# Performance work log

Measured on AMD Instinct MI355X. Metric: run time of the kernel, lower is better.

## Reference

```python
import jax, jax.numpy as jnp
import numpy as np

EMB, HEADS = 1024, 16
HEAD_DIM = EMB // HEADS


def _linear(x, W, b):
    # torch nn.Linear convention: x @ W.T + b, W: [out, in]
    return jnp.einsum('bse,oe->bso', x, W) + b


def setup_inputs() -> dict:
    key = jax.random.key(0)
    ks = jax.random.split(key, 11)
    B, S = 2, 2048
    sc = 1.0 / np.sqrt(EMB)
    inp = {
        'x': jax.random.normal(ks[0], (B, S, EMB), dtype=jnp.float32),
        'y': jax.random.normal(ks[1], (B, S, EMB), dtype=jnp.float32),
        'mask': jnp.ones((B, S, S), dtype=jnp.int32),
        'Wq': jax.random.normal(ks[2], (EMB, EMB), dtype=jnp.float32) * sc,
        'bq': jax.random.normal(ks[3], (EMB,), dtype=jnp.float32) * sc,
        'Wk': jax.random.normal(ks[4], (EMB, EMB), dtype=jnp.float32) * sc,
        'bk': jax.random.normal(ks[5], (EMB,), dtype=jnp.float32) * sc,
        'Wv': jax.random.normal(ks[6], (EMB, EMB), dtype=jnp.float32) * sc,
        'bv': jax.random.normal(ks[7], (EMB,), dtype=jnp.float32) * sc,
        'Wo': jax.random.normal(ks[8], (EMB, EMB), dtype=jnp.float32) * sc,
        'bo': jax.random.normal(ks[9], (EMB,), dtype=jnp.float32) * sc,
    }
    return inp


def reference(x, y, mask, Wq, bq, Wk, bk, Wv, bv, Wo, bo):
    B, S, _ = x.shape
    q = _linear(x, Wq, bq).reshape(B, S, HEADS, HEAD_DIM).transpose(0, 2, 1, 3)
    k = _linear(y, Wk, bk).reshape(B, -1, HEADS, HEAD_DIM).transpose(0, 2, 1, 3)
    v = _linear(y, Wv, bv).reshape(B, -1, HEADS, HEAD_DIM).transpose(0, 2, 1, 3)
    # scores: [B, H, Sq, Sk]
    score = jnp.einsum('bhqd,bhkd->bhqk', q, k) / jnp.sqrt(jnp.float32(HEAD_DIM))
    # NOTE: original torch code calls score.masked_fill(...) without assignment,
    # so the mask has no effect on the computation (faithfully ignored here).
    weights = jax.nn.softmax(score, axis=-1)
    attn = jnp.einsum('bhqk,bhkd->bhqd', weights, v)
    attn = attn.transpose(0, 2, 1, 3).reshape(B, S, EMB)
    # dropout is identity in eval mode
    return _linear(attn, Wo, bo)
```

## Files before the change

### kernel.cpp

```cpp
#include <hip/hip_runtime.h>
#include <cstdint>
#include <cstddef>

#define BB 2
#define SS 2048
#define EE 1024
#define HH 16
#define DD 64

typedef __attribute__((ext_vector_type(8))) short short8;
typedef __attribute__((ext_vector_type(4))) short shortx4;
typedef __attribute__((ext_vector_type(8))) unsigned short ushort8;
typedef __attribute__((ext_vector_type(4))) unsigned short ush4;
typedef __attribute__((ext_vector_type(4))) float floatx4;

#define MFMA32(a, b, c) __builtin_amdgcn_mfma_f32_16x16x32_bf16((a), (b), (c), 0, 0, 0)
#define MFMA16(a, b, c) __builtin_amdgcn_mfma_f32_16x16x16bf16_1k((a), (b), (c), 0, 0, 0)

#define QSCALE 0.18033688011112042f

#define G2L16(g, l)                                                        \
    __builtin_amdgcn_global_load_lds(                                      \
        (const __attribute__((address_space(1))) void*)(g),                \
        (__attribute__((address_space(3))) void*)(l), 16, 0, 0)

__device__ __forceinline__ unsigned short f2bf(float f) {
    unsigned int u = __float_as_uint(f);
    u += 0x7fffu + ((u >> 16) & 1u);
    return (unsigned short)(u >> 16);
}

__device__ __forceinline__ unsigned int pkbf(float a, float b) {
    return __builtin_amdgcn_perm(__float_as_uint(b) + 0x8000u,
                                 __float_as_uint(a) + 0x8000u, 0x07060302u);
}

__global__ __launch_bounds__(256) void k_cvt(
    const float* __restrict__ x, unsigned short* __restrict__ xb,
    const float* __restrict__ y, unsigned short* __restrict__ yb,
    const float* __restrict__ w0, unsigned short* __restrict__ d0,
    const float* __restrict__ w1, unsigned short* __restrict__ d1,
    const float* __restrict__ w2, unsigned short* __restrict__ d2,
    const float* __restrict__ w3, unsigned short* __restrict__ d3)
{
    const int g = blockIdx.y;
    if (g >= 2 && blockIdx.x >= 256) return;
    const float* s = (g == 0) ? x : (g == 1) ? y : (g == 2) ? w0
                   : (g == 3) ? w1 : (g == 4) ? w2 : w3;
    unsigned short* d = (g == 0) ? xb : (g == 1) ? yb : (g == 2) ? d0
                      : (g == 3) ? d1 : (g == 4) ? d2 : d3;
    const size_t i = ((size_t)blockIdx.x * 256 + threadIdx.x) * 16;
    floatx4 f0 = *(const floatx4*)(s + i);
    floatx4 f1 = *(const floatx4*)(s + i + 4);
    floatx4 f2 = *(const floatx4*)(s + i + 8);
    floatx4 f3 = *(const floatx4*)(s + i + 12);
    ushort8 o0, o1;
#pragma unroll
    for (int j = 0; j < 4; ++j) { o0[j] = f2bf(f0[j]); o0[j + 4] = f2bf(f1[j]); }
#pragma unroll
    for (int j = 0; j < 4; ++j) { o1[j] = f2bf(f2[j]); o1[j + 4] = f2bf(f3[j]); }
    *(ushort8*)(d + i) = o0;
    *(ushort8*)(d + i + 8) = o1;
}

template <int MT, int OMODE>
__device__ __forceinline__ void gemm_body(
    const unsigned short* __restrict__ A, const unsigned short* __restrict__ W,
    const float* __restrict__ bias, void* __restrict__ Cv, float oscale,
    int m0, int n0,
    unsigned short* As0, unsigned short* As1, unsigned short* As2,
    unsigned short* Bs0, unsigned short* Bs1, unsigned short* Bs2)
{
    constexpr int K = 1024, N = 1024, LDT = 32;
    constexpr int MFR = MT / 32;
    constexpr int KEEP = (MT == 128) ? 8 : 6;
    const int t = threadIdx.x;
    const int lane = t & 63, w = t >> 6;
    const int q = lane >> 4, c = lane & 15;
    const int wm = w & 1, wn = w >> 1;
    const int lr = lane >> 2, lc = (lane & 3) * 8;

    const unsigned short* gA0 = A + (size_t)(m0 + w * (MT / 4) + lr) * K + lc;
    const unsigned short* gA1 = gA0 + 16 * K;
    const unsigned short* gB0 = W + (size_t)(n0 + w * 32 + lr) * K + lc;
    const unsigned short* gB1 = gB0 + 16 * K;
    unsigned short* lA0 = As0 + (w * (MT / 4)) * LDT;
    unsigned short* lA1 = As1 + (w * (MT / 4)) * LDT;
    unsigned short* lA2 = As2 + (w * (MT / 4)) * LDT;
    unsigned short* lB0 = Bs0 + (w * 32) * LDT;
    unsigned short* lB1 = Bs1 + (w * 32) * LDT;
    unsigned short* lB2 = Bs2 + (w * 32) * LDT;

    floatx4 acc[MFR][4] = {};

    auto compute = [&](const unsigned short* Ah, const unsigned short* Bh) {
        short8 af[MFR], bfr[4];
#pragma unroll
        for (int mi = 0; mi < MFR; ++mi)
            af[mi] = *(const short8*)
                &Ah[(wm * (MFR * 16) + mi * 16 + c) * LDT + q * 8];
#pragma unroll
        for (int ni = 0; ni < 4; ++ni)
            bfr[ni] = *(const short8*)
                &Bh[(wn * 64 + ni * 16 + c) * LDT + q * 8];
#pragma unroll
        for (int mi = 0; mi < MFR; ++mi)
#pragma unroll
            for (int ni = 0; ni < 4; ++ni)
                acc[mi][ni] = MFMA32(af[mi], bfr[ni], acc[mi][ni]);
    };

    auto stage = [&](int nk, unsigned short* lA, unsigned short* lB) {
        G2L16(gA0 + nk, lA);
        if constexpr (MT == 128) G2L16(gA1 + nk, lA + 16 * LDT);
        G2L16(gB0 + nk, lB);
        G2L16(gB1 + nk, lB + 16 * LDT);
    };

    auto phase = [&](int knext, unsigned short* lAn, unsigned short* lBn,
                     const unsigned short* Ac, const unsigned short* Bc) {
        __builtin_amdgcn_s_barrier();
        stage(knext & (K - 1), lAn, lBn);
        asm volatile("s_waitcnt vmcnt(%0)" :: "n"(KEEP) : "memory");
        __builtin_amdgcn_s_barrier();
        __builtin_amdgcn_sched_barrier(0);
        compute(Ac, Bc);
    };

    stage(0, lA0, lB0);
    stage(32, lA1, lB1);

    for (int g = 0; g < 10; ++g) {
        const int kb = g * 96;
        phase(kb +  64, lA2, lB2, As0, Bs0);
        phase(kb +  96, lA0, lB0, As1, Bs1);
        phase(kb + 128, lA1, lB1, As2, Bs2);
    }
    phase(1056, lA2, lB2, As0, Bs0);
    phase(1088, lA0, lB0, As1, Bs1);
    asm volatile("s_waitcnt vmcnt(0)" ::: "memory");

#pragma unroll
    for (int ni = 0; ni < 4; ++ni) {
        const int col = n0 + wn * 64 + ni * 16 + c;
        const float bv = bias[col];
#pragma unroll
        for (int mi = 0; mi < MFR; ++mi)
#pragma unroll
            for (int r = 0; r < 4; ++r) {
                const int row = m0 + wm * (MFR * 16) + mi * 16 + q * 4 + r;
                const float v = (acc[mi][ni][r] + bv) * oscale;
                if constexpr (OMODE == 0) {
                    ((unsigned short*)Cv)[(size_t)row * N + col] = f2bf(v);
                } else if constexpr (OMODE == 1) {
                    const int b = row >> 11, s = row & 2047;
                    ((unsigned short*)Cv)[((size_t)(b * 1024 + col)) * SS + s] = f2bf(v);
                } else {
                    ((float*)Cv)[(size_t)row * N + col] = v;
                }
            }
    }
}

__global__ __launch_bounds__(256) void k_gemm_qkv(
    const unsigned short* __restrict__ x, const unsigned short* __restrict__ y,
    const unsigned short* __restrict__ Wq, const float* __restrict__ bq,
    const unsigned short* __restrict__ Wk, const float* __restrict__ bk,
    const unsigned short* __restrict__ Wv, const float* __restrict__ bv,
    unsigned short* __restrict__ Q, unsigned short* __restrict__ Ko,
    unsigned short* __restrict__ Vt)
{
    __shared__ __align__(16) unsigned short As0[128 * 32], As1[128 * 32],
                                            As2[128 * 32];
    __shared__ __align__(16) unsigned short Bs0[128 * 32], Bs1[128 * 32],
                                            Bs2[128 * 32];
    const int m0 = blockIdx.y * 128;
    const int nt = blockIdx.x;
    const int g = nt >> 3;
    const int n0 = (nt & 7) * 128;
    if (g == 0) {
        gemm_body<128, 0>(x, Wq, bq, Q, QSCALE, m0, n0,
                          As0, As1, As2, Bs0, Bs1, Bs2);
    } else if (g == 1) {
        gemm_body<128, 0>(y, Wk, bk, Ko, 1.0f, m0, n0,
                          As0, As1, As2, Bs0, Bs1, Bs2);
    } else {
        gemm_body<128, 1>(y, Wv, bv, Vt, 1.0f, m0, n0,
                          As0, As1, As2, Bs0, Bs1, Bs2);
    }
}

__global__ __launch_bounds__(256) void k_gemm_out(
    const unsigned short* __restrict__ A, const unsigned short* __restrict__ W,
    const float* __restrict__ bias, float* __restrict__ C)
{
    __shared__ __align__(16) unsigned short As0[128 * 32], As1[128 * 32],
                                            As2[128 * 32];
    __shared__ __align__(16) unsigned short Bs0[128 * 32], Bs1[128 * 32],
                                            Bs2[128 * 32];
    gemm_body<128, 2>(A, W, bias, C, 1.0f, blockIdx.y * 128, blockIdx.x * 128,
                      As0, As1, As2, Bs0, Bs1, Bs2);
}

__global__ __launch_bounds__(512, 4) void k_attn(
    const unsigned short* __restrict__ Q, const unsigned short* __restrict__ K,
    const unsigned short* __restrict__ Vt, unsigned short* __restrict__ O)
{
    constexpr int LDK = 72;
    constexpr int TSZ = 64 * LDK + 64 * 64;
    __shared__ __align__(16) unsigned short smem[2 * 2 * TSZ];
    float* Ob = (float*)smem;

    const int bh = blockIdx.x, qt = blockIdx.y;
    const int b = bh >> 4, h = bh & 15;
    const int t = threadIdx.x, w = t >> 6;
    const int ws = w >> 2;
    const int wq = w & 3;
    const int lane = t & 63, q = lane >> 4, c = lane & 15;

    unsigned short* Sb = smem + ws * (2 * TSZ);

    short8 qb[2][2];
#pragma unroll
    for (int g = 0; g < 2; ++g) {
        const size_t qoff =
            (size_t)(b * SS + qt * 128 + wq * 32 + g * 16 + c) * EE + h * DD + q * 8;
        qb[g][0] = *(const short8*)(Q + qoff);
        qb[g][1] = *(const short8*)(Q + qoff + 32);
    }

    floatx4 o[2][4] = {};
    floatx4 lacc[2] = {};
    const shortx4 ones = {(short)0x3F80, (short)0x3F80, (short)0x3F80, (short)0x3F80};

    const int ts = t & 255;
    const int sr = ts >> 2, sp = (ts & 3) * 16;
    const int vkey = (sr & 15) << 2;
    const unsigned short* Kg =
        K + (size_t)(b * SS + ws * 1024 + sr) * EE + h * DD + sp;
    const unsigned short* Vg =
        Vt + ((size_t)bh * DD + sr) * SS + ws * 1024 + sp;

    auto put = [&](unsigned short* Ks, unsigned short* Vs,
                   ushort8 k0, ushort8 k1, ushort8 v0, ushort8 v1) {
        *(ushort8*)&Ks[sr * LDK + sp] = k0;
        *(ushort8*)&Ks[sr * LDK + sp + 8] = k1;
        *(ush4*)&Vs[sr * 64 + ((sp +  0) ^ vkey)] =
            __builtin_shufflevector(v0, v0, 0, 1, 2, 3);
        *(ush4*)&Vs[sr * 64 + ((sp +  4) ^ vkey)] =
            __builtin_shufflevector(v0, v0, 4, 5, 6, 7);
        *(ush4*)&Vs[sr * 64 + ((sp +  8) ^ vkey)] =
            __builtin_shufflevector(v1, v1, 0, 1, 2, 3);
        *(ush4*)&Vs[sr * 64 + ((sp + 12) ^ vkey)] =
            __builtin_shufflevector(v1, v1, 4, 5, 6, 7);
    };

    ushort8 rk[2][2], rv[2][2];
    {
        const ushort8* gk0 = (const ushort8*)Kg;
        rk[0][0] = gk0[0]; rk[0][1] = gk0[1];
        const ushort8* gv0 = (const ushort8*)Vg;
        rv[0][0] = gv0[0]; rv[0][1] = gv0[1];
        const ushort8* gk1 = (const ushort8*)(Kg + (size_t)64 * EE);
        rk[1][0] = gk1[0]; rk[1][1] = gk1[1];
        const ushort8* gv1 = (const ushort8*)(Vg + 64);
        rv[1][0] = gv1[0]; rv[1][1] = gv1[1];
        put(Sb, Sb + 64 * LDK, rk[0][0], rk[0][1], rv[0][0], rv[0][1]);
        asm volatile("s_waitcnt lgkmcnt(0)" ::: "memory");
    }

#pragma unroll 2
    for (int it = 0; it < 16; ++it) {
        const unsigned short* Ks = Sb + (it & 1) * TSZ;
        const unsigned short* Vs = Ks + 64 * LDK;
        __builtin_amdgcn_s_barrier();
        __builtin_amdgcn_sched_barrier(0);

        {
            const int nit = (it + 2) & 15;
            const ushort8* gk = (const ushort8*)(Kg + (size_t)nit * 64 * EE);
            rk[it & 1][0] = gk[0]; rk[it & 1][1] = gk[1];
            const ushort8* gv = (const ushort8*)(Vg + nit * 64);
            rv[it & 1][0] = gv[0]; rv[it & 1][1] = gv[1];
        }

#pragma unroll
        for (int tt = 0; tt < 4; ++tt) {
            const short8 ka0 = *(const short8*)&Ks[(tt * 16 + c) * LDK + q * 8];
            const short8 ka1 = *(const short8*)&Ks[(tt * 16 + c) * LDK + 32 + q * 8];
            shortx4 pa[2];
#pragma unroll
            for (int g = 0; g < 2; ++g) {
                floatx4 s = {0.f, 0.f, 0.f, 0.f};
                s = MFMA32(ka0, qb[g][0], s);
                s = MFMA32(ka1, qb[g][1], s);
                union { unsigned int u[2]; shortx4 v; } pk;
                pk.u[0] = pkbf(__builtin_amdgcn_exp2f(s[0]),
                               __builtin_amdgcn_exp2f(s[1]));
                pk.u[1] = pkbf(__builtin_amdgcn_exp2f(s[2]),
                               __builtin_amdgcn_exp2f(s[3]));
                pa[g] = pk.v;
            }
#pragma unroll
            for (int nd = 0; nd < 4; ++nd) {
                const shortx4 vb = *(const shortx4*)
                    &Vs[(nd * 16 + c) * 64 + (((tt * 4 + q) ^ c) << 2)];
                o[0][nd] = MFMA16(pa[0], vb, o[0][nd]);
                o[1][nd] = MFMA16(pa[1], vb, o[1][nd]);
            }
            lacc[0] = MFMA16(pa[0], ones, lacc[0]);
            lacc[1] = MFMA16(pa[1], ones, lacc[1]);
        }

        __builtin_amdgcn_sched_barrier(0);
        {
            unsigned short* Kn = Sb + ((it + 1) & 1) * TSZ;
            unsigned short* Vn = Kn + 64 * LDK;
            put(Kn, Vn, rk[(it + 1) & 1][0], rk[(it + 1) & 1][1],
                rv[(it + 1) & 1][0], rv[(it + 1) & 1][1]);
        }
        asm volatile("s_waitcnt lgkmcnt(0)" ::: "memory");
    }

    __syncthreads();
    if (ws == 1) {
#pragma unroll
        for (int g = 0; g < 2; ++g) {
#pragma unroll
            for (int nd = 0; nd < 4; ++nd)
#pragma unroll
                for (int r = 0; r < 4; ++r)
                    Ob[(wq * 32 + g * 16 + q * 4 + r) * 66 + nd * 16 + c] =
                        o[g][nd][r];
            if (c == 0) {
#pragma unroll
                for (int r = 0; r < 4; ++r)
                    Ob[(wq * 32 + g * 16 + q * 4 + r) * 66 + 64] = lacc[g][r];
            }
        }
    }
    __syncthreads();
    if (ws == 0) {
#pragma unroll
        for (int g = 0; g < 2; ++g) {
            float linv[4];
#pragma unroll
            for (int r = 0; r < 4; ++r) {
                const int rr = wq * 32 + g * 16 + q * 4 + r;
#pragma unroll
                for (int nd = 0; nd < 4; ++nd)
                    o[g][nd][r] += Ob[rr * 66 + nd * 16 + c];
                linv[r] = __builtin_amdgcn_rcpf(lacc[g][r] + Ob[rr * 66 + 64]);
            }
            const int orow = b * SS + qt * 128 + wq * 32 + g * 16;
#pragma unroll
            for (int nd = 0; nd < 4; ++nd)
#pragma unroll
                for (int r = 0; r < 4; ++r)
                    O[(size_t)(orow + q * 4 + r) * EE + h * DD + nd * 16 + c] =
                        f2bf(o[g][nd][r] * linv[r]);
        }
    }
}

extern "C" void kernel_launch(void* const* d_in, const int* in_sizes, int n_in,
                              void* d_out, int out_size, void* d_ws, size_t ws_size,
                              hipStream_t stream)
{
    const float* x  = (const float*)d_in[0];
    const float* y  = (const float*)d_in[1];
    const float* Wq = (const float*)d_in[3];
    const float* bq = (const float*)d_in[4];
    const float* Wk = (const float*)d_in[5];
    const float* bk = (const float*)d_in[6];
    const float* Wv = (const float*)d_in[7];
    const float* bv = (const float*)d_in[8];
    const float* Wo = (const float*)d_in[9];
    const float* bo = (const float*)d_in[10];
    float* out = (float*)d_out;

    char* ws = (char*)d_ws;
    const size_t SZ = (size_t)BB * SS * EE * sizeof(unsigned short);
    const size_t WZ = (size_t)EE * EE * sizeof(unsigned short);
    unsigned short* xb  = (unsigned short*)(ws);
    unsigned short* yb  = (unsigned short*)(ws + SZ);
    unsigned short* Wqb = (unsigned short*)(ws + 2 * SZ);
    unsigned short* Wkb = (unsigned short*)(ws + 2 * SZ + WZ);
    unsigned short* Wvb = (unsigned short*)(ws + 2 * SZ + 2 * WZ);
    unsigned short* Wob = (unsigned short*)(ws + 2 * SZ + 3 * WZ);
    unsigned short* Qw  = (unsigned short*)(ws + 2 * SZ + 4 * WZ);
    unsigned short* Kw  = (unsigned short*)(ws + 3 * SZ + 4 * WZ);
    unsigned short* Vtw = (unsigned short*)(ws + 4 * SZ + 4 * WZ);
    unsigned short* Aw  = (unsigned short*)(ws + 5 * SZ + 4 * WZ);
    (void)ws_size; (void)in_sizes; (void)n_in; (void)out_size;

    k_cvt<<<dim3(1024, 6), 256, 0, stream>>>(x, xb, y, yb, Wq, Wqb, Wk, Wkb,
                                             Wv, Wvb, Wo, Wob);
    k_gemm_qkv<<<dim3(24, 32), 256, 0, stream>>>(xb, yb, Wqb, bq, Wkb, bk, Wvb, bv,
                                                 Qw, Kw, Vtw);
    k_attn<<<dim3(32, 16), 512, 0, stream>>>(Qw, Kw, Vtw, Aw);
    k_gemm_out<<<dim3(8, 32), 256, 0, stream>>>(Aw, Wob, bo, out);
}
```

Measured before the change: 229.9 us.

## Fuse fp32-to-bf16 conversion into GEMM loads and drop convert kernel

Removes the standalone conversion kernel and has the projection GEMMs read fp32 activations and weights directly, converting to bf16 in registers before writing to LDS. The staging changes from async global-to-LDS triple buffering to register-staged double buffering. This eliminates a full pass over inputs and weights and the bf16 intermediate buffers, at the cost of more global read bytes per GEMM, repeated weight conversion per tile, and a less asynchronous load pipeline.

```diff
diff --git a/kernel.cpp b/kernel.cpp
--- a/kernel.cpp
+++ b/kernel.cpp
@@ -19,11 +19,6 @@
 
 #define QSCALE 0.18033688011112042f
 
-#define G2L16(g, l)                                                        \
-    __builtin_amdgcn_global_load_lds(                                      \
-        (const __attribute__((address_space(1))) void*)(g),                \
-        (__attribute__((address_space(3))) void*)(l), 16, 0, 0)
-
 __device__ __forceinline__ unsigned short f2bf(float f) {
     unsigned int u = __float_as_uint(f);
     u += 0x7fffu + ((u >> 16) & 1u);
@@ -35,120 +30,105 @@
                                  __float_as_uint(a) + 0x8000u, 0x07060302u);
 }
 
-__global__ __launch_bounds__(256) void k_cvt(
-    const float* __restrict__ x, unsigned short* __restrict__ xb,
-    const float* __restrict__ y, unsigned short* __restrict__ yb,
-    const float* __restrict__ w0, unsigned short* __restrict__ d0,
-    const float* __restrict__ w1, unsigned short* __restrict__ d1,
-    const float* __restrict__ w2, unsigned short* __restrict__ d2,
-    const float* __restrict__ w3, unsigned short* __restrict__ d3)
-{
-    const int g = blockIdx.y;
-    if (g >= 2 && blockIdx.x >= 256) return;
-    const float* s = (g == 0) ? x : (g == 1) ? y : (g == 2) ? w0
-                   : (g == 3) ? w1 : (g == 4) ? w2 : w3;
-    unsigned short* d = (g == 0) ? xb : (g == 1) ? yb : (g == 2) ? d0
-                      : (g == 3) ? d1 : (g == 4) ? d2 : d3;
-    const size_t i = ((size_t)blockIdx.x * 256 + threadIdx.x) * 16;
-    floatx4 f0 = *(const floatx4*)(s + i);
-    floatx4 f1 = *(const floatx4*)(s + i + 4);
-    floatx4 f2 = *(const floatx4*)(s + i + 8);
-    floatx4 f3 = *(const floatx4*)(s + i + 12);
-    ushort8 o0, o1;
-#pragma unroll
-    for (int j = 0; j < 4; ++j) { o0[j] = f2bf(f0[j]); o0[j + 4] = f2bf(f1[j]); }
-#pragma unroll
-    for (int j = 0; j < 4; ++j) { o1[j] = f2bf(f2[j]); o1[j + 4] = f2bf(f3[j]); }
-    *(ushort8*)(d + i) = o0;
-    *(ushort8*)(d + i + 8) = o1;
-}
-
-template <int MT, int OMODE>
-__device__ __forceinline__ void gemm_body(
-    const unsigned short* __restrict__ A, const unsigned short* __restrict__ W,
+template <int OMODE, bool AF32>
+__device__ __forceinline__ void gemm_fused(
+    const void* __restrict__ Av, const float* __restrict__ W,
     const float* __restrict__ bias, void* __restrict__ Cv, float oscale,
-    int m0, int n0,
-    unsigned short* As0, unsigned short* As1, unsigned short* As2,
-    unsigned short* Bs0, unsigned short* Bs1, unsigned short* Bs2)
+    int m0, int n0, unsigned short* As0, unsigned short* As1,
+    unsigned short* Bs0, unsigned short* Bs1)
 {
     constexpr int K = 1024, N = 1024, LDT = 32;
-    constexpr int MFR = MT / 32;
-    constexpr int KEEP = (MT == 128) ? 8 : 6;
     const int t = threadIdx.x;
     const int lane = t & 63, w = t >> 6;
     const int q = lane >> 4, c = lane & 15;
     const int wm = w & 1, wn = w >> 1;
-    const int lr = lane >> 2, lc = (lane & 3) * 8;
-
-    const unsigned short* gA0 = A + (size_t)(m0 + w * (MT / 4) + lr) * K + lc;
-    const unsigned short* gA1 = gA0 + 16 * K;
-    const unsigned short* gB0 = W + (size_t)(n0 + w * 32 + lr) * K + lc;
-    const unsigned short* gB1 = gB0 + 16 * K;
-    unsigned short* lA0 = As0 + (w * (MT / 4)) * LDT;
-    unsigned short* lA1 = As1 + (w * (MT / 4)) * LDT;
-    unsigned short* lA2 = As2 + (w * (MT / 4)) * LDT;
-    unsigned short* lB0 = Bs0 + (w * 32) * LDT;
-    unsigned short* lB1 = Bs1 + (w * 32) * LDT;
-    unsigned short* lB2 = Bs2 + (w * 32) * LDT;
-
-    floatx4 acc[MFR][4] = {};
-
+    const int srow = t >> 1, sk = (t & 1) * 16;
+
+    const float* gAf = (const float*)Av + (size_t)(m0 + srow) * K + sk;
+    const unsigned short* gAh =
+        (const unsigned short*)Av + (size_t)(m0 + srow) * K + sk;
+    const float* gB = W + (size_t)(n0 + srow) * K + sk;
+    unsigned short* wA[2] = {As0 + srow * LDT + sk, As1 + srow * LDT + sk};
+    unsigned short* wB[2] = {Bs0 + srow * LDT + sk, Bs1 + srow * LDT + sk};
+
+    floatx4 acc[4][4] = {};
+    floatx4 rAf[2][4];
+    ushort8 rAh[2][2];
+    floatx4 rBf[2][4];
+
+    auto load = [&](int p, int s) {
+        const int np = p & 31;
+        if constexpr (AF32) {
+            const floatx4* g = (const floatx4*)(gAf + np * 32);
+            rAf[s][0] = g[0]; rAf[s][1] = g[1];
+            rAf[s][2] = g[2]; rAf[s][3] = g[3];
+        } else {
+            const ushort8* g = (const ushort8*)(gAh + np * 32);
+            rAh[s][0] = g[0]; rAh[s][1] = g[1];
+        }
+        const floatx4* gb = (const floatx4*)(gB + np * 32);
+        rBf[s][0] = gb[0]; rBf[s][1] = gb[1];
+        rBf[s][2] = gb[2]; rBf[s][3] = gb[3];
+    };
+    auto cv8 = [](floatx4 a, floatx4 b) {
+        ushort8 o;
+#pragma unroll
+        for (int j = 0; j < 4; ++j) { o[j] = f2bf(a[j]); o[j + 4] = f2bf(b[j]); }
+        return o;
+    };
+    auto put = [&](int s, int buf) {
+        if constexpr (AF32) {
+            *(ushort8*)wA[buf]       = cv8(rAf[s][0], rAf[s][1]);
+            *(ushort8*)(wA[buf] + 8) = cv8(rAf[s][2], rAf[s][3]);
+        } else {
+            *(ushort8*)wA[buf]       = rAh[s][0];
+            *(ushort8*)(wA[buf] + 8) = rAh[s][1];
+        }
+        *(ushort8*)wB[buf]       = cv8(rBf[s][0], rBf[s][1]);
+        *(ushort8*)(wB[buf] + 8) = cv8(rBf[s][2], rBf[s][3]);
+    };
     auto compute = [&](const unsigned short* Ah, const unsigned short* Bh) {
-        short8 af[MFR], bfr[4];
-#pragma unroll
-        for (int mi = 0; mi < MFR; ++mi)
+        short8 af[4], bfr[4];
+#pragma unroll
+        for (int mi = 0; mi < 4; ++mi)
             af[mi] = *(const short8*)
-                &Ah[(wm * (MFR * 16) + mi * 16 + c) * LDT + q * 8];
+                &Ah[(wm * 64 + mi * 16 + c) * LDT + q * 8];
 #pragma unroll
         for (int ni = 0; ni < 4; ++ni)
             bfr[ni] = *(const short8*)
                 &Bh[(wn * 64 + ni * 16 + c) * LDT + q * 8];
 #pragma unroll
-        for (int mi = 0; mi < MFR; ++mi)
+        for (int mi = 0; mi < 4; ++mi)
 #pragma unroll
             for (int ni = 0; ni < 4; ++ni)
                 acc[mi][ni] = MFMA32(af[mi], bfr[ni], acc[mi][ni]);
     };
 
-    auto stage = [&](int nk, unsigned short* lA, unsigned short* lB) {
-        G2L16(gA0 + nk, lA);
-        if constexpr (MT == 128) G2L16(gA1 + nk, lA + 16 * LDT);
-        G2L16(gB0 + nk, lB);
-        G2L16(gB1 + nk, lB + 16 * LDT);
-    };
-
-    auto phase = [&](int knext, unsigned short* lAn, unsigned short* lBn,
-                     const unsigned short* Ac, const unsigned short* Bc) {
-        __builtin_amdgcn_s_barrier();
-        stage(knext & (K - 1), lAn, lBn);
-        asm volatile("s_waitcnt vmcnt(%0)" :: "n"(KEEP) : "memory");
+    load(0, 0);
+    load(1, 1);
+    put(0, 0);
+    asm volatile("s_waitcnt lgkmcnt(0)" ::: "memory");
+
+#pragma unroll 2
+    for (int p = 0; p < 32; ++p) {
         __builtin_amdgcn_s_barrier();
         __builtin_amdgcn_sched_barrier(0);
-        compute(Ac, Bc);
-    };
-
-    stage(0, lA0, lB0);
-    stage(32, lA1, lB1);
-
-    for (int g = 0; g < 10; ++g) {
-        const int kb = g * 96;
-        phase(kb +  64, lA2, lB2, As0, Bs0);
-        phase(kb +  96, lA0, lB0, As1, Bs1);
-        phase(kb + 128, lA1, lB1, As2, Bs2);
-    }
-    phase(1056, lA2, lB2, As0, Bs0);
-    phase(1088, lA0, lB0, As1, Bs1);
-    asm volatile("s_waitcnt vmcnt(0)" ::: "memory");
+        load(p + 2, p & 1);
+        compute((p & 1) ? As1 : As0, (p & 1) ? Bs1 : Bs0);
+        __builtin_amdgcn_sched_barrier(0);
+        put((p + 1) & 1, (p + 1) & 1);
+        asm volatile("s_waitcnt lgkmcnt(0)" ::: "memory");
+    }
 
 #pragma unroll
     for (int ni = 0; ni < 4; ++ni) {
         const int col = n0 + wn * 64 + ni * 16 + c;
         const float bv = bias[col];
 #pragma unroll
-        for (int mi = 0; mi < MFR; ++mi)
+        for (int mi = 0; mi < 4; ++mi)
 #pragma unroll
             for (int r = 0; r < 4; ++r) {
-                const int row = m0 + wm * (MFR * 16) + mi * 16 + q * 4 + r;
+                const int row = m0 + wm * 64 + mi * 16 + q * 4 + r;
                 const float v = (acc[mi][ni][r] + bv) * oscale;
                 if constexpr (OMODE == 0) {
                     ((unsigned short*)Cv)[(size_t)row * N + col] = f2bf(v);
@@ -163,43 +143,36 @@
 }
 
 __global__ __launch_bounds__(256) void k_gemm_qkv(
-    const unsigned short* __restrict__ x, const unsigned short* __restrict__ y,
-    const unsigned short* __restrict__ Wq, const float* __restrict__ bq,
-    const unsigned short* __restrict__ Wk, const float* __restrict__ bk,
-    const unsigned short* __restrict__ Wv, const float* __restrict__ bv,
+    const float* __restrict__ x, const float* __restrict__ y,
+    const float* __restrict__ Wq, const float* __restrict__ bq,
+    const float* __restrict__ Wk, const float* __restrict__ bk,
+    const float* __restrict__ Wv, const float* __restrict__ bv,
     unsigned short* __restrict__ Q, unsigned short* __restrict__ Ko,
     unsigned short* __restrict__ Vt)
 {
-    __shared__ __align__(16) unsigned short As0[128 * 32], As1[128 * 32],
-                                            As2[128 * 32];
-    __shared__ __align__(16) unsigned short Bs0[128 * 32], Bs1[128 * 32],
-                                            Bs2[128 * 32];
+    __shared__ __align__(16) unsigned short As0[128 * 32], As1[128 * 32];
+    __shared__ __align__(16) unsigned short Bs0[128 * 32], Bs1[128 * 32];
     const int m0 = blockIdx.y * 128;
     const int nt = blockIdx.x;
     const int g = nt >> 3;
     const int n0 = (nt & 7) * 128;
     if (g == 0) {
-        gemm_body<128, 0>(x, Wq, bq, Q, QSCALE, m0, n0,
-                          As0, As1, As2, Bs0, Bs1, Bs2);
+        gemm_fused<0, true>(x, Wq, bq, Q, QSCALE, m0, n0, As0, As1, Bs0, Bs1);
     } else if (g == 1) {
-        gemm_body<128, 0>(y, Wk, bk, Ko, 1.0f, m0, n0,
-                          As0, As1, As2, Bs0, Bs1, Bs2);
+        gemm_fused<0, true>(y, Wk, bk, Ko, 1.0f, m0, n0, As0, As1, Bs0, Bs1);
     } else {
-        gemm_body<128, 1>(y, Wv, bv, Vt, 1.0f, m0, n0,
-                          As0, As1, As2, Bs0, Bs1, Bs2);
+        gemm_fused<1, true>(y, Wv, bv, Vt, 1.0f, m0, n0, As0, As1, Bs0, Bs1);
     }
 }
 
 __global__ __launch_bounds__(256) void k_gemm_out(
-    const unsigned short* __restrict__ A, const unsigned short* __restrict__ W,
+    const unsigned short* __restrict__ A, const float* __restrict__ W,
     const float* __restrict__ bias, float* __restrict__ C)
 {
-    __shared__ __align__(16) unsigned short As0[128 * 32], As1[128 * 32],
-                                            As2[128 * 32];
-    __shared__ __align__(16) unsigned short Bs0[128 * 32], Bs1[128 * 32],
-                                            Bs2[128 * 32];
-    gemm_body<128, 2>(A, W, bias, C, 1.0f, blockIdx.y * 128, blockIdx.x * 128,
-                      As0, As1, As2, Bs0, Bs1, Bs2);
+    __shared__ __align__(16) unsigned short As0[128 * 32], As1[128 * 32];
+    __shared__ __align__(16) unsigned short Bs0[128 * 32], Bs1[128 * 32];
+    gemm_fused<2, false>(A, W, bias, C, 1.0f, blockIdx.y * 128,
+                         blockIdx.x * 128, As0, As1, Bs0, Bs1);
 }
 
 __global__ __launch_bounds__(512, 4) void k_attn(
@@ -381,23 +354,14 @@
 
     char* ws = (char*)d_ws;
     const size_t SZ = (size_t)BB * SS * EE * sizeof(unsigned short);
-    const size_t WZ = (size_t)EE * EE * sizeof(unsigned short);
-    unsigned short* xb  = (unsigned short*)(ws);
-    unsigned short* yb  = (unsigned short*)(ws + SZ);
-    unsigned short* Wqb = (unsigned short*)(ws + 2 * SZ);
-    unsigned short* Wkb = (unsigned short*)(ws + 2 * SZ + WZ);
-    unsigned short* Wvb = (unsigned short*)(ws + 2 * SZ + 2 * WZ);
-    unsigned short* Wob = (unsigned short*)(ws + 2 * SZ + 3 * WZ);
-    unsigned short* Qw  = (unsigned short*)(ws + 2 * SZ + 4 * WZ);
-    unsigned short* Kw  = (unsigned short*)(ws + 3 * SZ + 4 * WZ);
-    unsigned short* Vtw = (unsigned short*)(ws + 4 * SZ + 4 * WZ);
-    unsigned short* Aw  = (unsigned short*)(ws + 5 * SZ + 4 * WZ);
+    unsigned short* Qw  = (unsigned short*)(ws);
+    unsigned short* Kw  = (unsigned short*)(ws + SZ);
+    unsigned short* Vtw = (unsigned short*)(ws + 2 * SZ);
+    unsigned short* Aw  = (unsigned short*)(ws + 3 * SZ);
     (void)ws_size; (void)in_sizes; (void)n_in; (void)out_size;
 
-    k_cvt<<<dim3(1024, 6), 256, 0, stream>>>(x, xb, y, yb, Wq, Wqb, Wk, Wkb,
-                                             Wv, Wvb, Wo, Wob);
-    k_gemm_qkv<<<dim3(24, 32), 256, 0, stream>>>(xb, yb, Wqb, bq, Wkb, bk, Wvb, bv,
+    k_gemm_qkv<<<dim3(24, 32), 256, 0, stream>>>(x, y, Wq, bq, Wk, bk, Wv, bv,
                                                  Qw, Kw, Vtw);
     k_attn<<<dim3(32, 16), 512, 0, stream>>>(Qw, Kw, Vtw, Aw);
-    k_gemm_out<<<dim3(8, 32), 256, 0, stream>>>(Aw, Wob, bo, out);
-}
+    k_gemm_out<<<dim3(8, 32), 256, 0, stream>>>(Aw, Wo, bo, out);
+}
```

Measured after the change: 247.4 us. +7.6%, slower.
